# Performance work log

Hardware: AMD Instinct MI355X
Metric: run time of the kernel (lower is better)

## Reference

```python
import jax, jax.numpy as jnp
import numpy as np

T = 2_097_152  # timesteps


def setup_inputs() -> dict:
    key = jax.random.key(0)
    # precipitation P and potential evapotranspiration E, in mm/day
    x = jax.random.uniform(key, (T, 2), dtype=jnp.float32) * 10.0
    x1 = jnp.float32(350.0)  # production store capacity (mm)
    return {"x": x, "x1": x1}


def reference(x, x1):
    # GR4J production storage. s_init = 0.0.
    P = x[:, 0]
    E = x[:, 1]
    p_n = jax.nn.relu(P - E)  # net rainfall
    e_n = jax.nn.relu(E - P)  # net evapotranspiration
    # tanh(p_n/x1), tanh(e_n/x1) only depend on inputs -> precompute (same math)
    t_p = jnp.tanh(p_n / x1)
    t_e = jnp.tanh(e_n / x1)
    s0 = jnp.float32(0.0) * x1  # s_init * x1

    def step(s, te):
        tp, tn = te
        r = s / x1
        p_s = x1 * (1.0 - r ** 2) * tp / (1.0 + r * tp)
        e_s = s * (2.0 - r) * tn / (1.0 + (1.0 - r) * tn)
        s = s + p_s - e_s
        perc = s * (1.0 - (1.0 + ((4.0 / 9.0) * s / x1) ** 4) ** (-0.25))
        s = s - perc
        return s, (p_s, perc, s)

    _, (p_s, perc, s_store) = jax.lax.scan(step, s0, (t_p, t_e))

    # concat([p_n[:,None], e_n[:,None], p_s[:,None], perc[:,None]], axis=1)
    out = jnp.stack([p_n, e_n, p_s, perc], axis=1)  # [T, 4]
    # scale=True with mu/sigma None: standardize with batch statistics
    mu = jnp.mean(out, axis=0)
    sigma = jnp.std(out, axis=0)  # population std, matches tf.math.reduce_std
    out = (out - mu) / sigma
    return out, s_store[:, None]
```

## Files before the change

### kernel.cpp

```cpp
#include <hip/hip_runtime.h>


typedef float f32x4 __attribute__((ext_vector_type(4)));

#define LCH      32
#define CPB      128
#define TPB      384
#define BSTEPS   4096
#define WUP      1536
#define WUMAP    96
#define WSTO     12
#define NMAP     352
#define HODD     176
#define NCK      129
#define NMST     4
#define NWAVE    6

#define CC1 0.98078528f
#define CC2 0.92387953f
#define CC3 0.83146961f
#define CC4 0.70710678f
#define CC5 0.55557023f
#define CC6 0.38268343f
#define CC7 0.19509032f

__device__ __forceinline__ void stepk(float& s, const f32x4 k, float gma) {
    float s2m = s * s;
    float t1  = fmaf(k.y, s, k.x);
    float t2  = fmaf(k.w, s, k.z);
    float s1  = fmaf(s2m, t2, t1);
    float w2  = s1 * s1;
    float q4  = gma * s1;
    float w4  = w2 * w2;
    s = fmaf(-q4, w4, s1);
}

__device__ __forceinline__ void stepk_m(float& s, const f32x4 k, float gma,
                                        float& ps_o, float& pc_o) {
    float sp  = s;
    float s2m = s * s;
    float t1  = fmaf(k.y, s, k.x);
    float t2  = fmaf(k.w, s, k.z);
    float s1  = fmaf(s2m, t2, t1);
    float w2  = s1 * s1;
    float q4  = gma * s1;
    float w4  = w2 * w2;
    s = fmaf(-q4, w4, s1);
    ps_o = fmaxf(s1 - sp, 0.0f);
    pc_o = q4 * w4;
}

struct KC { float inv, x1, x1sq, x1_2, two_x1cu, five_x1sq, four_x1; };

__device__ __forceinline__ f32x4 mkk(float P, float Ev, const KC c,
                                     float& pn_o, float& en_o) {
    float d  = P - Ev;
    float pn = fmaxf(d, 0.f), en = fmaxf(-d, 0.f);
    float up = pn * c.inv, un = en * c.inv;
    float tp = up * fmaf(up * up, -(1.f/3.f), 1.f);
    float tn = un * fmaf(un * un, -(1.f/3.f), 1.f);
    float al = tp * c.inv, be = tn * c.inv;
    float a2 = al * al,  a3v = a2 * al;
    float b2 = be * be,  b3v = b2 * be;
    float e2 = fmaf(-be, c.x1, 1.f);
    float k0 = tp * c.x1;
    float k1 = 1.f - a2 * c.x1sq - (c.x1_2 * be * e2 + c.two_x1cu * b3v);
    float k2 = (a3v * c.x1sq - al) - (c.x1_2 * b2 - be * e2 - c.five_x1sq * b3v);
    float k3 = a2 + b2 - c.four_x1 * b3v;
    pn_o = pn; en_o = en;
    return (f32x4){k0, k1, k2, k3};
}

__global__ __launch_bounds__(TPB, 3) void scan_h384(
        const float* __restrict__ x, const float* __restrict__ x1p,
        f32x4* __restrict__ pspc4, f32x4* __restrict__ s4,
        float* __restrict__ partials) {
    __shared__ f32x4 tk[32 * NCK];
    __shared__ f32x4 mapA[NMAP];
    __shared__ f32x4 mapB[NMAP];
    __shared__ float red[8 * NWAVE];

    const int tid  = threadIdx.x;
    const int lane = tid & 63;
    const int wid  = tid >> 6;
    const int b    = blockIdx.x;

    const float x1 = x1p[0];
    KC c;
    c.inv = 1.0f / x1; c.x1 = x1; c.x1sq = x1 * x1; c.x1_2 = 2.0f * x1;
    c.two_x1cu = 2.0f * x1 * c.x1sq; c.five_x1sq = 5.0f * c.x1sq;
    c.four_x1 = 4.0f * x1;
    const float gma = 64.0f / (6561.0f * c.x1sq * c.x1sq);
    const float cen = (184.0f / 350.0f) * x1;
    const float hw  = (208.0f / 350.0f) * x1;
    const float ihw = 1.0f / hw;

    float spn = 0.f, sen = 0.f, qpn = 0.f, qen = 0.f;

    if (tid < NMAP) {
        const f32x4* __restrict__ x4 = (const f32x4*)x;
        const f32x4 z4 = (f32x4){0.f, 0.f, 0.f, 0.f};
        const long gp = (long)b * (BSTEPS / 2) + 8L * (tid - WUMAP);
        f32x4 w[8];
        #pragma unroll
        for (int q = 0; q < 8; ++q) {
            const long g = gp + q;
            w[q] = (g >= 0) ? x4[g] : z4;
        }

        float snode[8];
        {
            const float ND[8] = { CC1,  CC3,  CC5,  CC7, -CC7, -CC5, -CC3, -CC1};
            #pragma unroll
            for (int j = 0; j < 8; ++j) snode[j] = fmaf(hw, ND[j], cen);
        }

        const int m = tid - WUMAP;
        const bool mainm = (m >= 0);
        float sv[8];
        #pragma unroll
        for (int j = 0; j < 8; ++j) sv[j] = snode[j];
        #pragma unroll
        for (int q = 0; q < 8; ++q) {
            float pn0, en0, pn1, en1;
            const f32x4 kA = mkk(w[q].x, w[q].y, c, pn0, en0);
            const f32x4 kB = mkk(w[q].z, w[q].w, c, pn1, en1);
            #pragma unroll
            for (int j = 0; j < 8; ++j) {
                stepk(sv[j], kA, gma);
                stepk(sv[j], kB, gma);
            }
            if (mainm) {
                spn += pn0 + pn1; sen += en0 + en1;
                qpn = fmaf(pn0, pn0, fmaf(pn1, pn1, qpn));
                qen = fmaf(en0, en0, fmaf(en1, en1, qen));
                const int t = 16 * m + 2 * q;
                const int r = t & 31, col = t >> 5;
                tk[r * NCK + col]       = kA;
                tk[(r + 1) * NCK + col] = kB;
            }
        }
        float v[8];
        #pragma unroll
        for (int j = 0; j < 8; ++j) v[j] = (sv[j] - cen) * ihw;
        const float e0 = v[0] + v[7], e1 = v[1] + v[6];
        const float e2 = v[2] + v[5], e3 = v[3] + v[4];
        const float o0 = v[0] - v[7], o1 = v[1] - v[6];
        const float o2 = v[2] - v[5], o3 = v[3] - v[4];
        const float a0 = 0.125f * (e0 + e1 + e2 + e3);
        const float a1 = 0.25f * (o0*CC1 + o1*CC3 + o2*CC5 + o3*CC7);
        const float a2 = 0.25f * ((e0 - e3)*CC2 + (e1 - e2)*CC6);
        const float a3 = 0.25f * (o0*CC3 - o1*CC7 - o2*CC1 - o3*CC5);
        const float a4 = 0.25f * CC4 * ((e0 + e3) - (e1 + e2));
        const float a5 = 0.25f * (o0*CC5 - o1*CC1 + o2*CC7 + o3*CC3);
        const float a6 = 0.25f * ((e0 - e3)*CC6 - (e1 - e2)*CC2);
        const float a7 = 0.25f * (o0*CC7 - o1*CC5 + o2*CC3 - o3*CC1);
        const int slot = (tid >> 1) + ((tid & 1) ? HODD : 0);
        mapA[slot] = (f32x4){a0 - a2 + a4 - a6,
                             a1 - 3.0f*a3 + 5.0f*a5 - 7.0f*a7,
                             2.0f*a2 - 8.0f*a4 + 18.0f*a6,
                             4.0f*a3 - 20.0f*a5 + 56.0f*a7};
        mapB[slot] = (f32x4){8.0f*a4 - 48.0f*a6,
                             16.0f*a5 - 112.0f*a7,
                             32.0f*a6,
                             64.0f*a7};
    }
    __syncthreads();

    float aps = 0.f, apc = 0.f, qps = 0.f, qpc = 0.f;
    float sg = 0.f;
    if (tid < CPB) {
        const int l = tid;
        const long gstart = ((long)b * CPB + l) * LCH;
        const float s0 = (gstart >= WUP) ? 0.47f * x1 : 0.0f;
        sg = (s0 - cen) * ihw;
        f32x4 A[8], B[8];
        #pragma unroll 1
        for (int st = 0; st < WSTO; ++st) {
            const int base = l + 4 * st;
            #pragma unroll
            for (int u = 0; u < 8; ++u)
                A[u] = mapA[base + (u >> 1) + ((u & 1) ? HODD : 0)];
            #pragma unroll
            for (int u = 0; u < 8; ++u)
                B[u] = mapB[base + (u >> 1) + ((u & 1) ? HODD : 0)];
            #pragma unroll
            for (int u = 0; u < 8; ++u) {
                const float s2  = sg * sg;
                const float p0  = fmaf(A[u].y, sg, A[u].x);
                const float p1  = fmaf(A[u].w, sg, A[u].z);
                const float p2  = fmaf(B[u].y, sg, B[u].x);
                const float p3  = fmaf(B[u].w, sg, B[u].z);
                const float s4v = s2 * s2;
                const float q0  = fmaf(p1, s2, p0);
                const float q1  = fmaf(p3, s2, p2);
                sg = fmaf(q1, s4v, q0);
            }
        }
    }
    const float s_after = fmaf(hw, sg, cen);

    if (tid < CPB) {
        const int l = tid;
        const size_t chunk = (size_t)b * CPB + l;
        float s = s_after;
        f32x4 K[8];
        #pragma unroll 1
        for (int m = 0; m < NMST; ++m) {
            const int base = (m << 3) * NCK + l;
            #pragma unroll
            for (int u = 0; u < 8; ++u) K[u] = tk[base + u * NCK];
            float psv[8], pcv[8], sv[8];
            #pragma unroll
            for (int u = 0; u < 8; ++u) {
                stepk_m(s, K[u], gma, psv[u], pcv[u]);
                sv[u] = s;
            }
            #pragma unroll
            for (int u = 0; u < 8; ++u) {
                aps += psv[u]; apc += pcv[u];
                qps = fmaf(psv[u], psv[u], qps); qpc = fmaf(pcv[u], pcv[u], qpc);
            }
            const size_t pb = chunk * 16 + 4 * m;
            pspc4[pb + 0] = (f32x4){psv[0], pcv[0], psv[1], pcv[1]};
            pspc4[pb + 1] = (f32x4){psv[2], pcv[2], psv[3], pcv[3]};
            pspc4[pb + 2] = (f32x4){psv[4], pcv[4], psv[5], pcv[5]};
            pspc4[pb + 3] = (f32x4){psv[6], pcv[6], psv[7], pcv[7]};
            const size_t sb = chunk * 8 + 2 * m;
            s4[sb]     = (f32x4){sv[0], sv[1], sv[2], sv[3]};
            s4[sb + 1] = (f32x4){sv[4], sv[5], sv[6], sv[7]};
        }
    }

    float vals[8] = {spn, sen, aps, apc, qpn, qen, qps, qpc};
    #pragma unroll
    for (int k = 0; k < 8; ++k) {
        float v = vals[k];
        #pragma unroll
        for (int off = 32; off > 0; off >>= 1) v += __shfl_down(v, off, 64);
        if (lane == 0) red[k * NWAVE + wid] = v;
    }
    __syncthreads();
    if (tid < 8) {
        float v = 0.f;
        #pragma unroll
        for (int wv = 0; wv < NWAVE; ++wv) v += red[tid * NWAVE + wv];
        partials[b * 8 + tid] = v;
    }
}

__global__ __launch_bounds__(256) void normalize_stats(
        const float* __restrict__ x, const f32x4* __restrict__ pspc4,
        const float* __restrict__ pA, f32x4* __restrict__ out4,
        int nA, int Thalf, int T) {
    __shared__ float red[256];
    __shared__ float sst[8];
    const int tid = threadIdx.x;
    {
        const int c = tid & 7;
        float v = 0.f;
        for (int i = tid >> 3; i < nA; i += 32) v += pA[i * 8 + c];
        red[tid] = v;
        __syncthreads();
        for (int off = 128; off >= 8; off >>= 1) {
            if (tid < off) red[tid] += red[tid + off];
            __syncthreads();
        }
        if (tid == 0) {
            const float invT = 1.0f / (float)T;
            #pragma unroll
            for (int k = 0; k < 4; ++k) {
                float mu  = red[k] * invT;
                float var = fmaxf(fmaf(-mu, mu, red[4 + k] * invT), 0.0f);
                sst[k]     = mu;
                sst[4 + k] = (var > 0.0f) ? rsqrtf(var) : 0.0f;
            }
        }
        __syncthreads();
    }
    const float mu0 = sst[0], mu1 = sst[1], mu2 = sst[2], mu3 = sst[3];
    const float is0 = sst[4], is1 = sst[5], is2 = sst[6], is3 = sst[7];
    const f32x4* __restrict__ x4 = (const f32x4*)x;
    for (int i = blockIdx.x * 256 + tid; i < Thalf; i += 1024 * 256) {
        f32x4 xv = x4[i];
        f32x4 pq = pspc4[i];
        float d0 = xv.x - xv.y, d1 = xv.z - xv.w;
        out4[2 * i]     = (f32x4){(fmaxf(d0, 0.f) - mu0) * is0,
                                  (fmaxf(-d0, 0.f) - mu1) * is1,
                                  (pq.x - mu2) * is2,
                                  (pq.y - mu3) * is3};
        out4[2 * i + 1] = (f32x4){(fmaxf(d1, 0.f) - mu0) * is0,
                                  (fmaxf(-d1, 0.f) - mu1) * is1,
                                  (pq.z - mu2) * is2,
                                  (pq.w - mu3) * is3};
    }
}

#define L_CHUNK  128
#define FB_WARMUP 2048
__device__ __forceinline__ float inv1p_fb(float a) {
    float i1 = 1.0f - a;
    float i2 = fmaf(-a, i1, 1.0f);
    return fmaf(-a, i2, 1.0f);
}
struct SCfb { float x1, inv_x1, c49; };
__device__ __forceinline__ void scan_step_fb(float& s, float P, float E, const SCfb c,
                                             float& pn, float& en, float& ps, float& pc) {
    float d = P - E;
    float pn_ = fmaxf(d, 0.0f), en_ = fmaxf(-d, 0.0f);
    float up = pn_ * c.inv_x1;
    float tp = up * fmaf(up * up, -(1.0f / 3.0f), 1.0f);
    float un = en_ * c.inv_x1;
    float tn = un * fmaf(un * un, -(1.0f / 3.0f), 1.0f);
    float r = s * c.inv_x1;
    float ps_ = (tp * c.x1) * fmaf(-r, r, 1.0f) * inv1p_fb(r * tp);
    float es_ = (s * (2.0f - r)) * tn * inv1p_fb((1.0f - r) * tn);
    float s1 = s + ps_ - es_;
    float z = s1 * c.c49, z2 = z * z, v = z2 * z2;
    float t = fmaf(v, fmaf(v, 0.15625f, -0.25f), 1.0f);
    float s2 = s1 * t;
    pn = pn_; en = en_; ps = ps_; pc = s1 - s2; s = s2;
}
__global__ __launch_bounds__(256) void scan_kernel_fb(
        const float* __restrict__ x, const float* __restrict__ x1ptr,
        float* __restrict__ out, float* __restrict__ s_store,
        float* __restrict__ partials, int T) {
    const int c = blockIdx.x * blockDim.x + threadIdx.x;
    const int nchunks = (T + L_CHUNK - 1) / L_CHUNK;
    SCfb cc; cc.x1 = x1ptr[0]; cc.inv_x1 = 1.0f / cc.x1; cc.c49 = (4.0f / 9.0f) * cc.inv_x1;
    float s1a[4] = {0.f, 0.f, 0.f, 0.f};
    float s2a[4] = {0.f, 0.f, 0.f, 0.f};
    if (c < nchunks) {
        const int g0 = c * L_CHUNK;
        const int g1 = min(g0 + L_CHUNK, T);
        const int w0 = max(g0 - FB_WARMUP, 0);
        float s = 0.0f; float pn, en, ps, pc;
        const float2* __restrict__ x2 = (const float2*)x;
        for (int t = w0; t < g0; ++t) { float2 xv = x2[t]; scan_step_fb(s, xv.x, xv.y, cc, pn, en, ps, pc); }
        float4* __restrict__ out4 = (float4*)out;
        for (int t = g0; t < g1; ++t) {
            float2 xv = x2[t];
            scan_step_fb(s, xv.x, xv.y, cc, pn, en, ps, pc);
            out4[t] = make_float4(pn, en, ps, pc);
            s_store[t] = s;
            s1a[0] += pn; s1a[1] += en; s1a[2] += ps; s1a[3] += pc;
            s2a[0] = fmaf(pn, pn, s2a[0]); s2a[1] = fmaf(en, en, s2a[1]);
            s2a[2] = fmaf(ps, ps, s2a[2]); s2a[3] = fmaf(pc, pc, s2a[3]);
        }
    }
    __shared__ float red[256];
    float vals[8] = {s1a[0], s1a[1], s1a[2], s1a[3], s2a[0], s2a[1], s2a[2], s2a[3]};
    for (int k = 0; k < 8; ++k) {
        red[threadIdx.x] = vals[k];
        __syncthreads();
        for (int off = 128; off > 0; off >>= 1) {
            if ((int)threadIdx.x < off) red[threadIdx.x] += red[threadIdx.x + off];
            __syncthreads();
        }
        if (threadIdx.x == 0) partials[blockIdx.x * 8 + k] = red[0];
        __syncthreads();
    }
}
__global__ __launch_bounds__(64) void finalize_fb(
        const float* __restrict__ partials, float* __restrict__ stats, int nblk, int T) {
    const int lane = threadIdx.x;
    float v[8] = {0.f, 0.f, 0.f, 0.f, 0.f, 0.f, 0.f, 0.f};
    for (int b = lane; b < nblk; b += 64)
        for (int k = 0; k < 8; ++k) v[k] += partials[b * 8 + k];
    #pragma unroll
    for (int k = 0; k < 8; ++k)
        for (int off = 32; off > 0; off >>= 1) v[k] += __shfl_down(v[k], off, 64);
    if (lane == 0) {
        const float invT = 1.0f / (float)T;
        for (int k = 0; k < 4; ++k) {
            float mu = v[k] * invT;
            float var = fmaxf(fmaf(-mu, mu, v[k + 4] * invT), 0.0f);
            stats[k] = mu;
            stats[4 + k] = (var > 0.0f) ? rsqrtf(var) : 0.0f;
        }
    }
}
__global__ __launch_bounds__(256) void normalize_fb(
        float* __restrict__ out, const float* __restrict__ stats, int T) {
    const int t = blockIdx.x * blockDim.x + threadIdx.x;
    if (t >= T) return;
    const float4 mu = *(const float4*)stats;
    const float4 is = *(const float4*)(stats + 4);
    float4* o4 = (float4*)out;
    float4 v = o4[t];
    v.x = (v.x - mu.x) * is.x; v.y = (v.y - mu.y) * is.y;
    v.z = (v.z - mu.z) * is.z; v.w = (v.w - mu.w) * is.w;
    o4[t] = v;
}

extern "C" void kernel_launch(void* const* d_in, const int* in_sizes, int n_in,
                              void* d_out, int out_size, void* d_ws, size_t ws_size,
                              hipStream_t stream) {
    const float* x  = (const float*)d_in[0];
    const float* x1 = (const float*)d_in[1];
    const int T = in_sizes[0] / 2;

    float* out     = (float*)d_out;
    float* s_store = out + 4 * (size_t)T;

    const int nblk = T / BSTEPS;

    float* pA = (float*)d_ws;
    const size_t pq_off = 4608;
    const size_t need = (pq_off + 2 * (size_t)T) * sizeof(float);

    const bool fast = (T % BSTEPS == 0) && nblk >= 1 && nblk <= 512 &&
                      (ws_size >= need);

    if (fast) {
        f32x4* pspc4 = (f32x4*)((float*)d_ws + pq_off);
        scan_h384<<<nblk, TPB, 0, stream>>>(x, x1, pspc4, (f32x4*)s_store, pA);
        normalize_stats<<<1024, 256, 0, stream>>>(x, pspc4, pA,
                                                  (f32x4*)out, nblk, T / 2, T);
    } else {
        float* stats    = (float*)d_ws;
        float* partials = stats + 8;
        const int nchunks = (T + L_CHUNK - 1) / L_CHUNK;
        const int nblkA = (nchunks + 255) / 256;
        scan_kernel_fb<<<nblkA, 256, 0, stream>>>(x, x1, out, s_store, partials, T);
        finalize_fb<<<1, 64, 0, stream>>>(partials, stats, nblkA, T);
        normalize_fb<<<(T + 255) / 256, 256, 0, stream>>>(out, stats, T);
    }
}
```

Measured before the change: 116.9 us.

## Write raw outputs from scan kernel and normalize in place

The scan kernel now writes the unnormalized [pn, en, ps, pc] rows straight into the output and accumulates all eight statistics in the scan threads, rereading x there. The normalize kernel becomes an in-place read-modify-write of the output. This drops the workspace ps/pc buffer and the second read of x. The block size also changes from 384 to 512 threads. The trade-offs are uncoalesced per-thread strided output stores in the scan phase, and a full read of the output in the second kernel in place of reading x plus the pspc buffer.

```diff
diff --git a/kernel.cpp b/kernel.cpp
--- a/kernel.cpp
+++ b/kernel.cpp
@@ -5,7 +5,7 @@
 
 #define LCH      32
 #define CPB      128
-#define TPB      384
+#define TPB      512
 #define BSTEPS   4096
 #define WUP      1536
 #define WUMAP    96
@@ -13,8 +13,7 @@
 #define NMAP     352
 #define HODD     176
 #define NCK      129
-#define NMST     4
-#define NWAVE    6
+#define NWAVE    8
 
 #define CC1 0.98078528f
 #define CC2 0.92387953f
@@ -52,8 +51,7 @@
 
 struct KC { float inv, x1, x1sq, x1_2, two_x1cu, five_x1sq, four_x1; };
 
-__device__ __forceinline__ f32x4 mkk(float P, float Ev, const KC c,
-                                     float& pn_o, float& en_o) {
+__device__ __forceinline__ f32x4 mkk(float P, float Ev, const KC c) {
     float d  = P - Ev;
     float pn = fmaxf(d, 0.f), en = fmaxf(-d, 0.f);
     float up = pn * c.inv, un = en * c.inv;
@@ -67,13 +65,12 @@
     float k1 = 1.f - a2 * c.x1sq - (c.x1_2 * be * e2 + c.two_x1cu * b3v);
     float k2 = (a3v * c.x1sq - al) - (c.x1_2 * b2 - be * e2 - c.five_x1sq * b3v);
     float k3 = a2 + b2 - c.four_x1 * b3v;
-    pn_o = pn; en_o = en;
     return (f32x4){k0, k1, k2, k3};
 }
 
-__global__ __launch_bounds__(TPB, 3) void scan_h384(
+__global__ __launch_bounds__(TPB, 4) void scan_fused(
         const float* __restrict__ x, const float* __restrict__ x1p,
-        f32x4* __restrict__ pspc4, f32x4* __restrict__ s4,
+        f32x4* __restrict__ out4, f32x4* __restrict__ s4,
         float* __restrict__ partials) {
     __shared__ f32x4 tk[32 * NCK];
     __shared__ f32x4 mapA[NMAP];
@@ -95,12 +92,12 @@
     const float hw  = (208.0f / 350.0f) * x1;
     const float ihw = 1.0f / hw;
 
-    float spn = 0.f, sen = 0.f, qpn = 0.f, qen = 0.f;
+    const f32x4* __restrict__ x4 = (const f32x4*)x;
 
     if (tid < NMAP) {
-        const f32x4* __restrict__ x4 = (const f32x4*)x;
         const f32x4 z4 = (f32x4){0.f, 0.f, 0.f, 0.f};
-        const long gp = (long)b * (BSTEPS / 2) + 8L * (tid - WUMAP);
+        const int m = tid - WUMAP;
+        const long gp = (long)b * 2048 + 8L * m;
         f32x4 w[8];
         #pragma unroll
         for (int q = 0; q < 8; ++q) {
@@ -108,36 +105,28 @@
             w[q] = (g >= 0) ? x4[g] : z4;
         }
 
-        float snode[8];
+        float sv[8];
         {
             const float ND[8] = { CC1,  CC3,  CC5,  CC7, -CC7, -CC5, -CC3, -CC1};
             #pragma unroll
-            for (int j = 0; j < 8; ++j) snode[j] = fmaf(hw, ND[j], cen);
-        }
-
-        const int m = tid - WUMAP;
+            for (int j = 0; j < 8; ++j) sv[j] = fmaf(hw, ND[j], cen);
+        }
         const bool mainm = (m >= 0);
-        float sv[8];
-        #pragma unroll
-        for (int j = 0; j < 8; ++j) sv[j] = snode[j];
+        const int  lcol  = m >> 1;
+        const int  rbase = (m & 1) << 4;
         #pragma unroll
         for (int q = 0; q < 8; ++q) {
-            float pn0, en0, pn1, en1;
-            const f32x4 kA = mkk(w[q].x, w[q].y, c, pn0, en0);
-            const f32x4 kB = mkk(w[q].z, w[q].w, c, pn1, en1);
+            const f32x4 kA = mkk(w[q].x, w[q].y, c);
+            const f32x4 kB = mkk(w[q].z, w[q].w, c);
             #pragma unroll
             for (int j = 0; j < 8; ++j) {
                 stepk(sv[j], kA, gma);
                 stepk(sv[j], kB, gma);
             }
             if (mainm) {
-                spn += pn0 + pn1; sen += en0 + en1;
-                qpn = fmaf(pn0, pn0, fmaf(pn1, pn1, qpn));
-                qen = fmaf(en0, en0, fmaf(en1, en1, qen));
-                const int t = 16 * m + 2 * q;
-                const int r = t & 31, col = t >> 5;
-                tk[r * NCK + col]       = kA;
-                tk[(r + 1) * NCK + col] = kB;
+                const int r = rbase + 2 * q;
+                tk[r * NCK + lcol]       = kA;
+                tk[(r + 1) * NCK + lcol] = kB;
             }
         }
         float v[8];
@@ -167,13 +156,14 @@
     }
     __syncthreads();
 
-    float aps = 0.f, apc = 0.f, qps = 0.f, qpc = 0.f;
-    float sg = 0.f;
+    float spn = 0.f, sen = 0.f, aps = 0.f, apc = 0.f;
+    float qpn = 0.f, qen = 0.f, qps = 0.f, qpc = 0.f;
     if (tid < CPB) {
         const int l = tid;
         const long gstart = ((long)b * CPB + l) * LCH;
         const float s0 = (gstart >= WUP) ? 0.47f * x1 : 0.0f;
-        sg = (s0 - cen) * ihw;
+        float sg = (s0 - cen) * ihw;
+
         f32x4 A[8], B[8];
         #pragma unroll 1
         for (int st = 0; st < WSTO; ++st) {
@@ -197,38 +187,36 @@
                 sg = fmaf(q1, s4v, q0);
             }
         }
-    }
-    const float s_after = fmaf(hw, sg, cen);
-
-    if (tid < CPB) {
-        const int l = tid;
+        float s = fmaf(hw, sg, cen);
+
         const size_t chunk = (size_t)b * CPB + l;
-        float s = s_after;
-        f32x4 K[8];
+        const long   P0    = (long)b * 2048 + 16L * l;
         #pragma unroll 1
-        for (int m = 0; m < NMST; ++m) {
-            const int base = (m << 3) * NCK + l;
-            #pragma unroll
-            for (int u = 0; u < 8; ++u) K[u] = tk[base + u * NCK];
-            float psv[8], pcv[8], sv[8];
+        for (int mst = 0; mst < 4; ++mst) {
+            f32x4 K[8];
+            const int rb = (mst << 3) * NCK + l;
+            #pragma unroll
+            for (int u = 0; u < 8; ++u) K[u] = tk[rb + u * NCK];
+            f32x4 xw[4];
+            #pragma unroll
+            for (int q = 0; q < 4; ++q) xw[q] = x4[P0 + 4 * mst + q];
+            float sv8[8];
             #pragma unroll
             for (int u = 0; u < 8; ++u) {
-                stepk_m(s, K[u], gma, psv[u], pcv[u]);
-                sv[u] = s;
+                float ps, pc;
+                stepk_m(s, K[u], gma, ps, pc);
+                sv8[u] = s;
+                const f32x4 wv = xw[u >> 1];
+                const float d  = (u & 1) ? (wv.z - wv.w) : (wv.x - wv.y);
+                const float pn = fmaxf(d, 0.f), en = fmaxf(-d, 0.f);
+                out4[chunk * 32 + 8 * mst + u] = (f32x4){pn, en, ps, pc};
+                spn += pn; sen += en; aps += ps; apc += pc;
+                qpn = fmaf(pn, pn, qpn); qen = fmaf(en, en, qen);
+                qps = fmaf(ps, ps, qps); qpc = fmaf(pc, pc, qpc);
             }
-            #pragma unroll
-            for (int u = 0; u < 8; ++u) {
-                aps += psv[u]; apc += pcv[u];
-                qps = fmaf(psv[u], psv[u], qps); qpc = fmaf(pcv[u], pcv[u], qpc);
-            }
-            const size_t pb = chunk * 16 + 4 * m;
-            pspc4[pb + 0] = (f32x4){psv[0], pcv[0], psv[1], pcv[1]};
-            pspc4[pb + 1] = (f32x4){psv[2], pcv[2], psv[3], pcv[3]};
-            pspc4[pb + 2] = (f32x4){psv[4], pcv[4], psv[5], pcv[5]};
-            pspc4[pb + 3] = (f32x4){psv[6], pcv[6], psv[7], pcv[7]};
-            const size_t sb = chunk * 8 + 2 * m;
-            s4[sb]     = (f32x4){sv[0], sv[1], sv[2], sv[3]};
-            s4[sb + 1] = (f32x4){sv[4], sv[5], sv[6], sv[7]};
+            const size_t sb = chunk * 8 + 2 * mst;
+            s4[sb]     = (f32x4){sv8[0], sv8[1], sv8[2], sv8[3]};
+            s4[sb + 1] = (f32x4){sv8[4], sv8[5], sv8[6], sv8[7]};
         }
     }
 
@@ -250,9 +238,8 @@
 }
 
 __global__ __launch_bounds__(256) void normalize_stats(
-        const float* __restrict__ x, const f32x4* __restrict__ pspc4,
         const float* __restrict__ pA, f32x4* __restrict__ out4,
-        int nA, int Thalf, int T) {
+        int nA, int T) {
     __shared__ float red[256];
     __shared__ float sst[8];
     const int tid = threadIdx.x;
@@ -280,19 +267,10 @@
     }
     const float mu0 = sst[0], mu1 = sst[1], mu2 = sst[2], mu3 = sst[3];
     const float is0 = sst[4], is1 = sst[5], is2 = sst[6], is3 = sst[7];
-    const f32x4* __restrict__ x4 = (const f32x4*)x;
-    for (int i = blockIdx.x * 256 + tid; i < Thalf; i += 1024 * 256) {
-        f32x4 xv = x4[i];
-        f32x4 pq = pspc4[i];
-        float d0 = xv.x - xv.y, d1 = xv.z - xv.w;
-        out4[2 * i]     = (f32x4){(fmaxf(d0, 0.f) - mu0) * is0,
-                                  (fmaxf(-d0, 0.f) - mu1) * is1,
-                                  (pq.x - mu2) * is2,
-                                  (pq.y - mu3) * is3};
-        out4[2 * i + 1] = (f32x4){(fmaxf(d1, 0.f) - mu0) * is0,
-                                  (fmaxf(-d1, 0.f) - mu1) * is1,
-                                  (pq.z - mu2) * is2,
-                                  (pq.w - mu3) * is3};
+    for (int i = blockIdx.x * 256 + tid; i < T; i += 1024 * 256) {
+        f32x4 v = out4[i];
+        out4[i] = (f32x4){(v.x - mu0) * is0, (v.y - mu1) * is1,
+                          (v.z - mu2) * is2, (v.w - mu3) * is3};
     }
 }
 
@@ -406,17 +384,15 @@
     const int nblk = T / BSTEPS;
 
     float* pA = (float*)d_ws;
-    const size_t pq_off = 4608;
-    const size_t need = (pq_off + 2 * (size_t)T) * sizeof(float);
+    const size_t need = 8192 * sizeof(float);
 
     const bool fast = (T % BSTEPS == 0) && nblk >= 1 && nblk <= 512 &&
                       (ws_size >= need);
 
     if (fast) {
-        f32x4* pspc4 = (f32x4*)((float*)d_ws + pq_off);
-        scan_h384<<<nblk, TPB, 0, stream>>>(x, x1, pspc4, (f32x4*)s_store, pA);
-        normalize_stats<<<1024, 256, 0, stream>>>(x, pspc4, pA,
-                                                  (f32x4*)out, nblk, T / 2, T);
+        scan_fused<<<nblk, TPB, 0, stream>>>(x, x1, (f32x4*)out,
+                                             (f32x4*)s_store, pA);
+        normalize_stats<<<1024, 256, 0, stream>>>(pA, (f32x4*)out, nblk, T);
     } else {
         float* stats    = (float*)d_ws;
         float* partials = stats + 8;
```

New measurement: 111.0 us. 1.05x faster.
